# Optimization experiments

Hardware: AMD Instinct MI355X
Metric: run time of the kernel (lower is better)

## Reference

```python
import jax, jax.numpy as jnp
import numpy as np

B, S, D = 4, 2048, 1024


def setup_inputs() -> dict:
    key = jax.random.key(0)
    ks = jax.random.split(key, 7)
    s = 1.0 / np.sqrt(D)
    return {
        "x": jax.random.normal(ks[0], (B, S, D), dtype=jnp.float32),
        "Wq": jax.random.normal(ks[1], (D, D), dtype=jnp.float32) * s,
        "bq": jax.random.normal(ks[2], (D,), dtype=jnp.float32) * s,
        "Wk": jax.random.normal(ks[3], (D, D), dtype=jnp.float32) * s,
        "bk": jax.random.normal(ks[4], (D,), dtype=jnp.float32) * s,
        "Wv": jax.random.normal(ks[5], (D, D), dtype=jnp.float32) * s,
        "bv": jax.random.normal(ks[6], (D,), dtype=jnp.float32) * s,
    }


def reference(x, Wq, bq, Wk, bk, Wv, bv):
    # Linear layers: y = x @ W^T + b (torch nn.Linear convention)
    Q = jnp.einsum("bsd,ed->bse", x, Wq) + bq  # [B,S,D]
    K = jnp.einsum("bsd,ed->bse", x, Wk) + bk
    V = jnp.einsum("bsd,ed->bse", x, Wv) + bv
    d = x.shape[-1]
    scores = jnp.einsum("bqd,bkd->bqk", Q, K) / jnp.sqrt(jnp.float32(d))  # [B,S,S]
    weights = jax.nn.softmax(scores, axis=-1)
    O = jnp.einsum("bqk,bkd->bqd", weights, V)  # [B,S,D]
    return O
```

## Files before the change

kernel.cpp:

```cpp
#include <hip/hip_runtime.h>

typedef __bf16    bf16x8 __attribute__((ext_vector_type(8)));
typedef __bf16    bf16x4 __attribute__((ext_vector_type(4)));
typedef float     f32x4  __attribute__((ext_vector_type(4)));

#define BM 128
#define BN 128
#define BK 64

__device__ __forceinline__ void gload_lds16(const __bf16* g, __bf16* l) {
  __builtin_amdgcn_global_load_lds(
      (const __attribute__((address_space(1))) void*)g,
      (__attribute__((address_space(3))) void*)l,
      16, 0, 0);
}

__global__ void cvt_all(const float* __restrict__ x, const float* __restrict__ Wq,
                        const float* __restrict__ Wk, const float* __restrict__ Wv,
                        __bf16* __restrict__ xb, __bf16* __restrict__ Wqk,
                        __bf16* __restrict__ Wvb, float* __restrict__ lsum) {
  int b = blockIdx.x;
  if (b == 0) {
    for (int j = threadIdx.x; j < 8192; j += 256) lsum[j] = 0.f;
  }
  const float* src;
  __bf16* dst;
  int i;
  if (b < 8192) {
    src = x; dst = xb; i = b * 256 + threadIdx.x;
  } else {
    b -= 8192;
    const int mat = b >> 10;
    i = (b & 1023) * 256 + threadIdx.x;
    src = (mat == 0) ? Wq : (mat == 1) ? Wk : Wv;
    dst = (mat == 0) ? Wqk : (mat == 1) ? (Wqk + 1048576) : Wvb;
  }
  float4 v = ((const float4*)src)[i];
  bf16x4 o;
  o[0] = (__bf16)v.x; o[1] = (__bf16)v.y; o[2] = (__bf16)v.z; o[3] = (__bf16)v.w;
  ((bf16x4*)dst)[i] = o;
}

template<int MODE>
__global__ __launch_bounds__(256, 2)
void gemm_bt(const __bf16* __restrict__ A, const __bf16* __restrict__ B,
             float* __restrict__ C,
             int lda, int ldb, int ldc, int K,
             long sA, long sB, long sC,
             const float* __restrict__ bias0, const float* __restrict__ bias1,
             float* __restrict__ lsum,
             __bf16* __restrict__ out0, __bf16* __restrict__ out1)
{
  A += (long)blockIdx.z * sA;
  B += (long)blockIdx.z * sB;

  const int tid  = threadIdx.x;
  const int wave = tid >> 6;
  const int lane = tid & 63;
  const int quad = lane >> 4;
  const int l15  = lane & 15;
  const int bm0  = blockIdx.x * BM;
  const int bn0  = blockIdx.y * BN;
  const int wm   = (wave >> 1) * 64;
  const int wn   = (wave & 1) * 64;

  __shared__ __align__(16) __bf16 As[BM * BK];
  __shared__ __align__(16) __bf16 Bs[BN * BK];

  f32x4 acc[4][4];
#pragma unroll
  for (int i = 0; i < 4; ++i)
#pragma unroll
    for (int j = 0; j < 4; ++j)
      acc[i][j] = (f32x4){0.f, 0.f, 0.f, 0.f};

  const __bf16* Ag[4];
  const __bf16* Bg[4];
#pragma unroll
  for (int c = 0; c < 4; ++c) {
    const int r  = c * 32 + (tid >> 3);
    const int g  = (tid & 7) ^ (r & 7);
    Ag[c] = A + (size_t)(bm0 + r) * lda + g * 8;
    Bg[c] = B + (size_t)(bn0 + r) * ldb + g * 8;
  }

  for (int k0 = 0; k0 < K; k0 += BK) {
#pragma unroll
    for (int c = 0; c < 4; ++c) {
      gload_lds16(Ag[c] + k0, &As[c * 2048 + tid * 8]);
      gload_lds16(Bg[c] + k0, &Bs[c * 2048 + tid * 8]);
    }
    __syncthreads();

#pragma unroll
    for (int kk = 0; kk < 2; ++kk) {
      bf16x8 af[4], bfv[4];
#pragma unroll
      for (int i = 0; i < 4; ++i) {
        const int R = wm + i * 16 + l15;
        af[i] = *(const bf16x8*)&As[R * BK + (((kk * 4 + quad) ^ (R & 7)) * 8)];
      }
#pragma unroll
      for (int i = 0; i < 4; ++i) {
        const int R = wn + i * 16 + l15;
        bfv[i] = *(const bf16x8*)&Bs[R * BK + (((kk * 4 + quad) ^ (R & 7)) * 8)];
      }
#pragma unroll
      for (int mi = 0; mi < 4; ++mi)
#pragma unroll
        for (int ni = 0; ni < 4; ++ni)
          acc[mi][ni] = __builtin_amdgcn_mfma_f32_16x16x32_bf16(
              af[mi], bfv[ni], acc[mi][ni], 0, 0, 0);
    }
    __syncthreads();
  }

  if (MODE == 2) {
#pragma unroll
    for (int mi = 0; mi < 4; ++mi) {
#pragma unroll
      for (int r = 0; r < 4; ++r) {
        const int gm = bm0 + wm + mi * 16 + quad * 4 + r;
        float part = 0.f;
#pragma unroll
        for (int ni = 0; ni < 4; ++ni) {
          const int gn = bn0 + wn + ni * 16 + l15;
          const __bf16 eb = (__bf16)__expf(acc[mi][ni][r] * 0.03125f);
          out0[(long)blockIdx.z * sC + (size_t)gm * ldc + gn] = eb;
          part += (float)eb;
        }
        part += __shfl_xor(part, 1);
        part += __shfl_xor(part, 2);
        part += __shfl_xor(part, 4);
        part += __shfl_xor(part, 8);
        if (l15 == 0)
          atomicAdd(&lsum[blockIdx.z * 2048 + gm], part);
      }
    }
  } else if (MODE == 3) {
#pragma unroll
    for (int mi = 0; mi < 4; ++mi) {
#pragma unroll
      for (int r = 0; r < 4; ++r) {
        const int gm = bm0 + wm + mi * 16 + quad * 4 + r;
        const float rv = 1.0f / lsum[blockIdx.z * 2048 + gm];
#pragma unroll
        for (int ni = 0; ni < 4; ++ni) {
          const int gn = bn0 + wn + ni * 16 + l15;
          C[(long)blockIdx.z * sC + (size_t)gm * ldc + gn] = acc[mi][ni][r] * rv;
        }
      }
    }
  } else {
#pragma unroll
    for (int mi = 0; mi < 4; ++mi) {
#pragma unroll
      for (int ni = 0; ni < 4; ++ni) {
        const int gn = bn0 + wn + ni * 16 + l15;
#pragma unroll
        for (int r = 0; r < 4; ++r) {
          const int gm = bm0 + wm + mi * 16 + quad * 4 + r;
          float v = acc[mi][ni][r];
          if (MODE == 0) {
            const int mat = gn >> 10;
            const int d   = gn & 1023;
            const float* bias = (mat == 0) ? bias0 : bias1;
            __bf16* dst = (mat == 0) ? out0 : out1;
            dst[(size_t)gm * 1024 + d] = (__bf16)(v + bias[d]);
          } else {
            const int b = gn >> 11, s = gn & 2047;
            out0[(size_t)b * (1024 * 2048) + (size_t)gm * 2048 + s] =
                (__bf16)(v + bias0[gm]);
          }
        }
      }
    }
  }
}

extern "C" void kernel_launch(void* const* d_in, const int* in_sizes, int n_in,
                              void* d_out, int out_size, void* d_ws, size_t ws_size,
                              hipStream_t stream) {
  const float* x  = (const float*)d_in[0];
  const float* Wq = (const float*)d_in[1];
  const float* bq = (const float*)d_in[2];
  const float* Wk = (const float*)d_in[3];
  const float* bk = (const float*)d_in[4];
  const float* Wv = (const float*)d_in[5];
  const float* bv = (const float*)d_in[6];
  float* out = (float*)d_out;

  char* ws = (char*)d_ws;
  __bf16* Q    = (__bf16*)(ws);
  __bf16* Kb   = (__bf16*)(ws + (16ull << 20));
  __bf16* Vt   = (__bf16*)(ws + (32ull << 20));
  __bf16* xb   = (__bf16*)(ws + (48ull << 20));
  __bf16* Wqk  = (__bf16*)(ws + (64ull << 20));
  __bf16* Wvb  = (__bf16*)(ws + (68ull << 20));
  __bf16* Sc   = (__bf16*)(ws + (48ull << 20));
  float*  lsum = (float*)(ws + (110ull << 20));

  dim3 blk(256);

  cvt_all<<<11264, blk, 0, stream>>>(x, Wq, Wk, Wv, xb, Wqk, Wvb, lsum);

  gemm_bt<0><<<dim3(64, 16, 1), blk, 0, stream>>>(
      xb, Wqk, nullptr, 1024, 1024, 0, 1024,
      0L, 0L, 0L, bq, bk, nullptr, Q, Kb);

  gemm_bt<1><<<dim3(8, 64, 1), blk, 0, stream>>>(
      Wvb, xb, nullptr, 1024, 1024, 0, 1024,
      0L, 0L, 0L, bv, nullptr, nullptr, Vt, nullptr);

  gemm_bt<2><<<dim3(16, 16, 4), blk, 0, stream>>>(
      Q, Kb, nullptr, 1024, 1024, 2048, 1024,
      2048L * 1024, 2048L * 1024, 2048L * 2048,
      nullptr, nullptr, lsum, Sc, nullptr);

  gemm_bt<3><<<dim3(16, 8, 4), blk, 0, stream>>>(
      Sc, Vt, out, 2048, 2048, 1024, 2048,
      2048L * 2048, 1024L * 2048, 2048L * 1024,
      nullptr, nullptr, lsum, nullptr, nullptr);
}
```

Before: 251.0 us.

## Add 256x256 multi-stage pipelined GEMM for QK projection and score kernels

Adds a new 512-thread GEMM kernel with 256x256 tiles, a 4-deep LDS ring of K=32 slices loaded with async global-to-LDS copies, explicit vmcnt waits and barriers, s_setprio around the MFMA bursts, and an XCD-aware remap of workgroup indices. It replaces the old 128x128 kernel for the fused Q/K projection and for the exp-score GEMM, aiming to raise data reuse per tile and overlap loads with MFMA work. The larger tiles produce far fewer workgroups (256 per launch) and need more registers and LDS per block, which may leave parts of the GPU underused. The hand-managed waitcnt counts must exactly match the issued loads.

```diff
diff --git a/kernel.cpp b/kernel.cpp
--- a/kernel.cpp
+++ b/kernel.cpp
@@ -39,6 +39,165 @@
   bf16x4 o;
   o[0] = (__bf16)v.x; o[1] = (__bf16)v.y; o[2] = (__bf16)v.z; o[3] = (__bf16)v.w;
   ((bf16x4*)dst)[i] = o;
+}
+
+template<int MODE>
+__global__ __launch_bounds__(512, 2)
+void gemm256(const __bf16* __restrict__ A, const __bf16* __restrict__ B,
+             int lda, int ldb, int ldc, int K,
+             long sA, long sB, long sC,
+             const float* __restrict__ bias0, const float* __restrict__ bias1,
+             float* __restrict__ lsum,
+             __bf16* __restrict__ out0, __bf16* __restrict__ out1)
+{
+  const int nwg = gridDim.x * gridDim.y * gridDim.z;
+  int lin = blockIdx.x + gridDim.x * (blockIdx.y + gridDim.y * blockIdx.z);
+  lin = (lin & 7) * (nwg >> 3) + (lin >> 3);
+  const int bx = lin % gridDim.x;
+  const int rest = lin / gridDim.x;
+  const int by = rest % gridDim.y;
+  const int bz = rest / gridDim.y;
+
+  A += (long)bz * sA;
+  B += (long)bz * sB;
+
+  const int tid  = threadIdx.x;
+  const int wave = tid >> 6;
+  const int lane = tid & 63;
+  const int quad = lane >> 4;
+  const int l15  = lane & 15;
+  const int bm0  = bx * 256;
+  const int bn0  = by * 256;
+  const int wm   = (wave >> 2) * 128;
+  const int wn   = (wave & 3) * 64;
+
+  __shared__ __align__(16) __bf16 As[4 * 8192];
+  __shared__ __align__(16) __bf16 Bs[4 * 8192];
+
+  f32x4 acc[8][4];
+#pragma unroll
+  for (int i = 0; i < 8; ++i)
+#pragma unroll
+    for (int j = 0; j < 4; ++j)
+      acc[i][j] = (f32x4){0.f, 0.f, 0.f, 0.f};
+
+  const int NH = K >> 5;
+
+  const int r0 = tid >> 2;
+  const int g0 = (tid & 3) ^ (r0 & 3);
+  const __bf16* A0 = A + (size_t)(bm0 + r0) * lda + g0 * 8;
+  const __bf16* A1 = A + (size_t)(bm0 + r0 + 128) * lda + g0 * 8;
+  const __bf16* B0 = B + (size_t)(bn0 + r0) * ldb + g0 * 8;
+  const __bf16* B1 = B + (size_t)(bn0 + r0 + 128) * ldb + g0 * 8;
+
+  auto stageU = [&](int u) {
+    const int s = u >> 1;
+    if (s < NH) {
+      if (u & 1) {
+        __bf16* d = &Bs[(s & 3) * 8192 + tid * 8];
+        gload_lds16(B0 + s * 32, d);
+        gload_lds16(B1 + s * 32, d + 4096);
+      } else {
+        __bf16* d = &As[(s & 3) * 8192 + tid * 8];
+        gload_lds16(A0 + s * 32, d);
+        gload_lds16(A1 + s * 32, d + 4096);
+      }
+    }
+  };
+
+  const int gq   = (quad ^ (l15 & 3)) * 8;
+  const int aoff = (wm + l15) * 32 + gq;
+  const int boff = (wn + l15) * 32 + gq;
+
+  stageU(0); stageU(1); stageU(2); stageU(3);
+  asm volatile("s_waitcnt vmcnt(4)" ::: "memory");
+  stageU(4); stageU(5); stageU(6);
+  asm volatile("s_waitcnt vmcnt(6)" ::: "memory");
+  __builtin_amdgcn_s_barrier();
+  __builtin_amdgcn_sched_barrier(0);
+
+  for (int h = 0; h < NH; ++h) {
+    const int P = (h & 3) * 8192;
+    bf16x8 af[4], bfv[4];
+#pragma unroll
+    for (int ni = 0; ni < 4; ++ni)
+      bfv[ni] = *(const bf16x8*)&Bs[P + ni * 512 + boff];
+#pragma unroll
+    for (int mi = 0; mi < 4; ++mi)
+      af[mi] = *(const bf16x8*)&As[P + mi * 512 + aoff];
+    stageU(2 * h + 7);
+    __builtin_amdgcn_s_barrier();
+    __builtin_amdgcn_s_setprio(1);
+#pragma unroll
+    for (int mi = 0; mi < 4; ++mi)
+#pragma unroll
+      for (int ni = 0; ni < 4; ++ni)
+        acc[mi][ni] = __builtin_amdgcn_mfma_f32_16x16x32_bf16(
+            af[mi], bfv[ni], acc[mi][ni], 0, 0, 0);
+    __builtin_amdgcn_s_setprio(0);
+    __builtin_amdgcn_s_barrier();
+#pragma unroll
+    for (int mi = 0; mi < 4; ++mi)
+      af[mi] = *(const bf16x8*)&As[P + 2048 + mi * 512 + aoff];
+    stageU(2 * h + 8);
+    __builtin_amdgcn_s_barrier();
+    __builtin_amdgcn_s_setprio(1);
+#pragma unroll
+    for (int mi = 0; mi < 4; ++mi)
+#pragma unroll
+      for (int ni = 0; ni < 4; ++ni)
+        acc[mi + 4][ni] = __builtin_amdgcn_mfma_f32_16x16x32_bf16(
+            af[mi], bfv[ni], acc[mi + 4][ni], 0, 0, 0);
+    __builtin_amdgcn_s_setprio(0);
+    if (h & 1) {
+      if (h + 4 < NH) asm volatile("s_waitcnt vmcnt(6)" ::: "memory");
+      else            asm volatile("s_waitcnt vmcnt(0)" ::: "memory");
+    }
+    __builtin_amdgcn_s_barrier();
+    if (h & 1) __builtin_amdgcn_sched_barrier(0);
+  }
+
+  if (MODE == 2) {
+    const long zc = (long)bz * sC;
+#pragma unroll
+    for (int mi = 0; mi < 8; ++mi) {
+#pragma unroll
+      for (int r = 0; r < 4; ++r) {
+        const int gm = bm0 + wm + mi * 16 + quad * 4 + r;
+        float part = 0.f;
+#pragma unroll
+        for (int ni = 0; ni < 4; ++ni) {
+          const int gn = bn0 + wn + ni * 16 + l15;
+          const __bf16 eb = (__bf16)__expf(acc[mi][ni][r] * 0.03125f);
+          out0[zc + (size_t)gm * ldc + gn] = eb;
+          part += (float)eb;
+        }
+        part += __shfl_xor(part, 1);
+        part += __shfl_xor(part, 2);
+        part += __shfl_xor(part, 4);
+        part += __shfl_xor(part, 8);
+        if (l15 == 0)
+          atomicAdd(&lsum[bz * 2048 + gm], part);
+      }
+    }
+  } else {
+#pragma unroll
+    for (int mi = 0; mi < 8; ++mi) {
+#pragma unroll
+      for (int ni = 0; ni < 4; ++ni) {
+        const int gn  = bn0 + wn + ni * 16 + l15;
+        const int mat = gn >> 10;
+        const int d   = gn & 1023;
+        const float* bias = (mat == 0) ? bias0 : bias1;
+        __bf16* dst = (mat == 0) ? out0 : out1;
+#pragma unroll
+        for (int r = 0; r < 4; ++r) {
+          const int gm = bm0 + wm + mi * 16 + quad * 4 + r;
+          dst[(size_t)gm * 1024 + d] = (__bf16)(acc[mi][ni][r] + bias[d]);
+        }
+      }
+    }
+  }
 }
 
 template<int MODE>
@@ -115,29 +274,7 @@
     __syncthreads();
   }
 
-  if (MODE == 2) {
-#pragma unroll
-    for (int mi = 0; mi < 4; ++mi) {
-#pragma unroll
-      for (int r = 0; r < 4; ++r) {
-        const int gm = bm0 + wm + mi * 16 + quad * 4 + r;
-        float part = 0.f;
-#pragma unroll
-        for (int ni = 0; ni < 4; ++ni) {
-          const int gn = bn0 + wn + ni * 16 + l15;
-          const __bf16 eb = (__bf16)__expf(acc[mi][ni][r] * 0.03125f);
-          out0[(long)blockIdx.z * sC + (size_t)gm * ldc + gn] = eb;
-          part += (float)eb;
-        }
-        part += __shfl_xor(part, 1);
-        part += __shfl_xor(part, 2);
-        part += __shfl_xor(part, 4);
-        part += __shfl_xor(part, 8);
-        if (l15 == 0)
-          atomicAdd(&lsum[blockIdx.z * 2048 + gm], part);
-      }
-    }
-  } else if (MODE == 3) {
+  if (MODE == 3) {
 #pragma unroll
     for (int mi = 0; mi < 4; ++mi) {
 #pragma unroll
@@ -160,18 +297,9 @@
 #pragma unroll
         for (int r = 0; r < 4; ++r) {
           const int gm = bm0 + wm + mi * 16 + quad * 4 + r;
-          float v = acc[mi][ni][r];
-          if (MODE == 0) {
-            const int mat = gn >> 10;
-            const int d   = gn & 1023;
-            const float* bias = (mat == 0) ? bias0 : bias1;
-            __bf16* dst = (mat == 0) ? out0 : out1;
-            dst[(size_t)gm * 1024 + d] = (__bf16)(v + bias[d]);
-          } else {
-            const int b = gn >> 11, s = gn & 2047;
-            out0[(size_t)b * (1024 * 2048) + (size_t)gm * 2048 + s] =
-                (__bf16)(v + bias0[gm]);
-          }
+          const int b = gn >> 11, s = gn & 2047;
+          out0[(size_t)b * (1024 * 2048) + (size_t)gm * 2048 + s] =
+              (__bf16)(acc[mi][ni][r] + bias0[gm]);
         }
       }
     }
@@ -200,24 +328,22 @@
   __bf16* Sc   = (__bf16*)(ws + (48ull << 20));
   float*  lsum = (float*)(ws + (110ull << 20));
 
-  dim3 blk(256);
-
-  cvt_all<<<11264, blk, 0, stream>>>(x, Wq, Wk, Wv, xb, Wqk, Wvb, lsum);
-
-  gemm_bt<0><<<dim3(64, 16, 1), blk, 0, stream>>>(
-      xb, Wqk, nullptr, 1024, 1024, 0, 1024,
+  cvt_all<<<11264, dim3(256), 0, stream>>>(x, Wq, Wk, Wv, xb, Wqk, Wvb, lsum);
+
+  gemm256<0><<<dim3(32, 8, 1), dim3(512), 0, stream>>>(
+      xb, Wqk, 1024, 1024, 1024, 1024,
       0L, 0L, 0L, bq, bk, nullptr, Q, Kb);
 
-  gemm_bt<1><<<dim3(8, 64, 1), blk, 0, stream>>>(
+  gemm_bt<1><<<dim3(8, 64, 1), dim3(256), 0, stream>>>(
       Wvb, xb, nullptr, 1024, 1024, 0, 1024,
       0L, 0L, 0L, bv, nullptr, nullptr, Vt, nullptr);
 
-  gemm_bt<2><<<dim3(16, 16, 4), blk, 0, stream>>>(
-      Q, Kb, nullptr, 1024, 1024, 2048, 1024,
+  gemm256<2><<<dim3(8, 8, 4), dim3(512), 0, stream>>>(
+      Q, Kb, 1024, 1024, 2048, 1024,
       2048L * 1024, 2048L * 1024, 2048L * 2048,
       nullptr, nullptr, lsum, Sc, nullptr);
 
-  gemm_bt<3><<<dim3(16, 8, 4), blk, 0, stream>>>(
+  gemm_bt<3><<<dim3(16, 8, 4), dim3(256), 0, stream>>>(
       Sc, Vt, out, 2048, 2048, 1024, 2048,
       2048L * 2048, 1024L * 2048, 2048L * 1024,
       nullptr, nullptr, lsum, nullptr, nullptr);
```

New measurement: 250.1 us. Within noise of the previous version (-0.4%).
